# Performance work log

Measured on AMD Instinct MI355X. Metric: run time of the kernel, lower is better.

The kernel has to match this reference:

```python
import jax, jax.numpy as jnp
import numpy as np
import math


def _selective_scan(u, delta, A, Bs, Cs, D, delta_bias):
    """Mamba selective scan.
    u, delta: (B,K,Dn,L); A: (K,Dn,N); Bs, Cs: (B,K,N,L); D, delta_bias: (K,Dn).
    delta_softplus=True semantics from selective_scan_fn.
    """
    delta = jax.nn.softplus(delta + delta_bias[None, :, :, None])
    dl = jnp.moveaxis(delta, -1, 0)  # (L,B,K,Dn)
    ul = jnp.moveaxis(u, -1, 0)      # (L,B,K,Dn)
    bl = jnp.moveaxis(Bs, -1, 0)     # (L,B,K,N)
    cl = jnp.moveaxis(Cs, -1, 0)     # (L,B,K,N)
    h0 = jnp.zeros(u.shape[:3] + (A.shape[-1],), u.dtype)  # (B,K,Dn,N)

    def step(h, inp):
        d, ut, bt, ct = inp
        h = jnp.exp(d[..., None] * A) * h + (d * ut)[..., None] * bt[:, :, None, :]
        y = jnp.einsum('bkdn,bkn->bkd', h, ct)
        return h, y

    _, ys = jax.lax.scan(step, h0, (dl, ul, bl, cl))
    return jnp.moveaxis(ys, 0, -1) + D[None, :, :, None] * u  # (B,K,Dn,L)


def setup_inputs() -> dict:
    key = jax.random.key(0)
    B, H, W, C = 8, 64, 64, 192
    Dn, N, R, K = 192, 8, 12, 4
    ks = jax.random.split(key, 8)
    x = jax.random.normal(ks[0], (B, H, W, C), jnp.float32)
    in_proj_w = jax.random.normal(ks[1], (2 * Dn, C), jnp.float32) * (C ** -0.5)
    conv_w = jax.random.normal(ks[2], (Dn, 1, 3, 3), jnp.float32) * 0.2
    conv_b = jnp.zeros((Dn,), jnp.float32)
    x_proj_w = jax.random.normal(ks[3], (K, R + 2 * N, Dn), jnp.float32) * (Dn ** -0.5)
    dt_std = R ** -0.5
    dt_projs_w = jax.random.uniform(ks[4], (K, Dn, R), jnp.float32, -dt_std, dt_std)
    dt = jnp.exp(jax.random.uniform(ks[5], (K, Dn), jnp.float32)
                 * (math.log(0.1) - math.log(0.001)) + math.log(0.001))
    dt = jnp.clip(dt, 1e-4, None)
    dt_projs_b = dt + jnp.log(-jnp.expm1(-dt))  # inverse softplus
    A_logs = jnp.broadcast_to(jnp.log(jnp.arange(1, N + 1, dtype=jnp.float32)), (K, Dn, N)).copy()
    Ds = jnp.ones((K, Dn), jnp.float32)
    ln_w = jnp.ones((Dn,), jnp.float32)
    ln_b = jnp.zeros((Dn,), jnp.float32)
    out_proj_w = jax.random.normal(ks[6], (C, Dn), jnp.float32) * (Dn ** -0.5)
    return {"x": x, "in_proj_w": in_proj_w, "conv_w": conv_w, "conv_b": conv_b,
            "x_proj_w": x_proj_w, "dt_projs_w": dt_projs_w, "dt_projs_b": dt_projs_b,
            "A_logs": A_logs, "Ds": Ds, "ln_w": ln_w, "ln_b": ln_b,
            "out_proj_w": out_proj_w}


def reference(x, in_proj_w, conv_w, conv_b, x_proj_w, dt_projs_w, dt_projs_b,
              A_logs, Ds, ln_w, ln_b, out_proj_w):
    B, H, W, C = x.shape
    K, _, Dn = x_proj_w.shape
    N = A_logs.shape[-1]
    R = dt_projs_w.shape[-1]
    L = H * W

    xz = x @ in_proj_w.T                       # (B,H,W,2*Dn)
    xf, z = jnp.split(xz, 2, axis=-1)
    xc = jnp.transpose(xf, (0, 3, 1, 2))       # (B,Dn,H,W)
    xc = jax.lax.conv_general_dilated(
        xc, conv_w, (1, 1), [(1, 1), (1, 1)],
        feature_group_count=Dn,
        dimension_numbers=('NCHW', 'OIHW', 'NCHW')) + conv_b[None, :, None, None]
    xc = jax.nn.silu(xc)

    # 4-directional scan sequences: hw, wh, reversed-hw, reversed-wh
    x_hw = xc.reshape(B, Dn, L)
    x_wh = jnp.transpose(xc, (0, 1, 3, 2)).reshape(B, Dn, L)
    x2 = jnp.stack([x_hw, x_wh], axis=1)
    xs = jnp.concatenate([x2, jnp.flip(x2, axis=-1)], axis=1)  # (B,4,Dn,L)

    x_dbl = jnp.einsum('bkdl,kcd->bkcl', xs, x_proj_w)
    dts, Bsx, Csx = jnp.split(x_dbl, [R, R + N], axis=2)
    dts = jnp.einsum('bkrl,kdr->bkdl', dts, dt_projs_w)

    A = -jnp.exp(A_logs)                       # (K,Dn,N)
    out_y = _selective_scan(xs, dts, A, Bsx, Csx, Ds, dt_projs_b)  # (B,4,Dn,L)

    inv_y = jnp.flip(out_y[:, 2:4], axis=-1)
    wh_y = jnp.transpose(out_y[:, 1].reshape(B, Dn, W, H), (0, 1, 3, 2)).reshape(B, Dn, L)
    invwh_y = jnp.transpose(inv_y[:, 1].reshape(B, Dn, W, H), (0, 1, 3, 2)).reshape(B, Dn, L)
    y = out_y[:, 0] + inv_y[:, 0] + wh_y + invwh_y  # (B,Dn,L)

    y = jnp.transpose(y, (0, 2, 1)).reshape(B, H, W, Dn)
    mu = y.mean(-1, keepdims=True)
    var = y.var(-1, keepdims=True)
    y = (y - mu) / jnp.sqrt(var + 1e-5) * ln_w + ln_b
    y = y * jax.nn.silu(z)
    return y @ out_proj_w.T
```

## Files before the change

### kernel.cpp

```cpp
#include <hip/hip_runtime.h>
#include <hip/hip_bf16.h>

constexpr int B_  = 8;
constexpr int H_  = 64;
constexpr int W_  = 64;
constexpr int C_  = 192;
constexpr int Dn  = 192;
constexpr int Nst = 8;
constexpr int R_  = 12;
constexpr int K_  = 4;
constexpr int L_  = H_ * W_;
constexpr int CS  = 32;
constexpr int NC  = L_ / CS;
constexpr int CPROJ = R_ + 2 * Nst;
constexpr int MROWS = B_ * L_;

typedef __attribute__((ext_vector_type(8))) short short8v;
typedef __attribute__((ext_vector_type(4))) float f32x4;

__device__ __forceinline__ int map_t(int k, int t) {
    int tt = (k >= 2) ? (L_ - 1 - t) : t;
    if (k & 1) tt = (tt & 63) * 64 + (tt >> 6);
    return tt;
}

__device__ __forceinline__ short f2bf(float f) {
    unsigned u = __float_as_uint(f);
    u += 0x7FFFu + ((u >> 16) & 1u);
    return (short)(u >> 16);
}
__device__ __forceinline__ float bf2f(short s) {
    return __uint_as_float(((unsigned)(unsigned short)s) << 16);
}

constexpr int WOFF_IN  = 0;
constexpr int WOFF_XP  = 73728;
constexpr int WOFF_OUT = 95232;
constexpr int WTOTAL   = 132096;
constexpr int XUNITS   = MROWS * Dn / 8;
constexpr int WUNITS   = WTOTAL / 8;
__global__ __launch_bounds__(256) void k_cvt(const float* __restrict__ x,
                                             const float* __restrict__ w_in,
                                             const float* __restrict__ xpw,
                                             const float* __restrict__ wout,
                                             short* __restrict__ x_bf,
                                             short* __restrict__ w_bf) {
    int g = blockIdx.x * 256 + threadIdx.x;
    const float* src;
    short* dst;
    int off;
    if (g < XUNITS) { src = x; dst = x_bf; off = g * 8; }
    else {
        g -= XUNITS;
        if (g >= WUNITS) return;
        int base = g * 8;
        dst = w_bf; off = base;
        if (base < WOFF_XP)       { src = w_in; }
        else if (base < WOFF_OUT) { src = xpw;  src -= WOFF_XP; }
        else                      { src = wout; src -= WOFF_OUT; }
    }
    float4 a = *reinterpret_cast<const float4*>(src + off);
    float4 b = *reinterpret_cast<const float4*>(src + off + 4);
    short8v v = {f2bf(a.x), f2bf(a.y), f2bf(a.z), f2bf(a.w),
                 f2bf(b.x), f2bf(b.y), f2bf(b.z), f2bf(b.w)};
    *reinterpret_cast<short8v*>(dst + off) = v;
}

__device__ __forceinline__ void mgemm_core(const short* __restrict__ A,
                                           const short* __restrict__ Wb,
                                           f32x4 (&acc)[4][2],
                                           int mrow, int ncol, int Nact, int K) {
    const int lane = threadIdx.x & 63;
    const int koff = (lane >> 4) * 8;
    for (int k0 = 0; k0 < K; k0 += 32) {
        short8v af[4], bfr[2];
#pragma unroll
        for (int mf = 0; mf < 4; mf++)
            af[mf] = *reinterpret_cast<const short8v*>(
                A + (size_t)(mrow + mf * 16) * K + k0 + koff);
#pragma unroll
        for (int nf = 0; nf < 2; nf++) {
            int r = ncol + nf * 16;
            short8v z = {0, 0, 0, 0, 0, 0, 0, 0};
            bfr[nf] = (r < Nact)
                ? *reinterpret_cast<const short8v*>(Wb + (size_t)r * K + k0 + koff)
                : z;
        }
#pragma unroll
        for (int mf = 0; mf < 4; mf++)
#pragma unroll
            for (int nf = 0; nf < 2; nf++)
                acc[mf][nf] = __builtin_amdgcn_mfma_f32_16x16x32_bf16(
                    af[mf], bfr[nf], acc[mf][nf], 0, 0, 0);
    }
}

__global__ __launch_bounds__(256) void k_mgemm_f(const short* __restrict__ A,
                                                 const short* __restrict__ Wb,
                                                 float* __restrict__ out0,
                                                 int Nact, int K) {
    const int m0 = blockIdx.x * 128, n0 = blockIdx.y * 64;
    const int wid = threadIdx.x >> 6, lane = threadIdx.x & 63;
    const int wm = wid >> 1, wn = wid & 1;
    f32x4 acc[4][2] = {};
    mgemm_core(A, Wb, acc, m0 + wm * 64 + (lane & 15), n0 + wn * 32 + (lane & 15),
               Nact, K);
    const int prow = (lane >> 4) * 4, pcol = lane & 15;
#pragma unroll
    for (int mf = 0; mf < 4; mf++) {
        int mbase = m0 + wm * 64 + mf * 16 + prow;
#pragma unroll
        for (int nf = 0; nf < 2; nf++) {
            int n = n0 + wn * 32 + nf * 16 + pcol;
            if (n >= Nact) continue;
#pragma unroll
            for (int r = 0; r < 4; r++)
                out0[(size_t)(mbase + r) * Nact + n] = acc[mf][nf][r];
        }
    }
}

__global__ __launch_bounds__(256) void k_mgemm_in(const short* __restrict__ A,
                                                  const short* __restrict__ Wb,
                                                  short* __restrict__ xf_bf,
                                                  short* __restrict__ z_bf,
                                                  int K) {
    const int m0 = blockIdx.x * 128, n0 = blockIdx.y * 64;
    const int wid = threadIdx.x >> 6, lane = threadIdx.x & 63;
    const int wm = wid >> 1, wn = wid & 1;
    f32x4 acc[4][2] = {};
    mgemm_core(A, Wb, acc, m0 + wm * 64 + (lane & 15), n0 + wn * 32 + (lane & 15),
               384, K);
    const int prow = (lane >> 4) * 4, pcol = lane & 15;
#pragma unroll
    for (int mf = 0; mf < 4; mf++) {
        int mbase = m0 + wm * 64 + mf * 16 + prow;
#pragma unroll
        for (int nf = 0; nf < 2; nf++) {
            int n = n0 + wn * 32 + nf * 16 + pcol;
#pragma unroll
            for (int r = 0; r < 4; r++) {
                int m = mbase + r;
                if (n < 192) xf_bf[(size_t)m * 192 + n] = f2bf(acc[mf][nf][r]);
                else         z_bf[(size_t)m * 192 + (n - 192)] = f2bf(acc[mf][nf][r]);
            }
        }
    }
}

__global__ __launch_bounds__(256) void k_conv(const short* __restrict__ xfb,
                                              const float* __restrict__ cw,
                                              const float* __restrict__ cb,
                                              short* __restrict__ xcb) {
    size_t i = (size_t)blockIdx.x * 256 + threadIdx.x;
    int d = (int)(i % Dn);
    int p = (int)(i / Dn);
    int w = p & 63; p >>= 6;
    int h = p & 63; p >>= 6;
    int b = p;
    float acc = cb[d];
#pragma unroll
    for (int kh = 0; kh < 3; kh++) {
        int hh = h + kh - 1;
        if (hh < 0 || hh >= H_) continue;
#pragma unroll
        for (int kw = 0; kw < 3; kw++) {
            int ww = w + kw - 1;
            if (ww < 0 || ww >= W_) continue;
            acc = fmaf(bf2f(xfb[(((size_t)b * H_ + hh) * W_ + ww) * Dn + d]),
                       cw[d * 9 + kh * 3 + kw], acc);
        }
    }
    float sig = 1.f / (1.f + __expf(-acc));
    xcb[i] = f2bf(acc * sig);
}

__device__ __forceinline__ void delta_e1(float x, float& delta, float& e1) {
    if (x > 20.f) { delta = x; e1 = __expf(-x); }
    else {
        float t = __expf(x);
        delta = __logf(1.f + t);
        e1 = __builtin_amdgcn_rcpf(1.f + t);
    }
}

__device__ __forceinline__ float dot12(const float4& a, const float4& b,
                                       const float4& c, const float* w, float x) {
    x = fmaf(a.x, w[0], x);  x = fmaf(a.y, w[1], x);
    x = fmaf(a.z, w[2], x);  x = fmaf(a.w, w[3], x);
    x = fmaf(b.x, w[4], x);  x = fmaf(b.y, w[5], x);
    x = fmaf(b.z, w[6], x);  x = fmaf(b.w, w[7], x);
    x = fmaf(c.x, w[8], x);  x = fmaf(c.y, w[9], x);
    x = fmaf(c.z, w[10], x); x = fmaf(c.w, w[11], x);
    return x;
}

__global__ __launch_bounds__(192) void k_scan1(const short* __restrict__ xcb,
                                               const float* __restrict__ xdbl,
                                               const float* __restrict__ dtw_all,
                                               const float* __restrict__ dtb_all,
                                               const float* __restrict__ alog,
                                               float* __restrict__ Aprod,
                                               float* __restrict__ hpart) {
    const int blk = blockIdx.x;
    const int c = blk % NC;
    const int k = (blk / NC) % K_;
    const int b = blk / (NC * K_);
    const int d = threadIdx.x;
    const int t0 = c * CS;
    const int stride = ((k & 1) ? 64 : 1) * ((k >= 2) ? -1 : 1);
    const int lm0 = map_t(k, t0);

    __shared__ float4 sx4[CS][5];
    const float4* xd4 = reinterpret_cast<const float4*>(xdbl);
    for (int i = d; i < CS * 5; i += 192) {
        int ts = i / 5, q = i % 5;
        sx4[ts][q] = xd4[((size_t)b * L_ + lm0 + ts * stride) * 28 + k * 7 + q];
    }
    __syncthreads();

    float dtw[R_];
#pragma unroll
    for (int r = 0; r < R_; r++) dtw[r] = dtw_all[((size_t)k * Dn + d) * R_ + r];
    const float bias = dtb_all[k * Dn + d];
    float Av[Nst];
    bool fast = true;
#pragma unroll
    for (int n = 0; n < Nst; n++) {
        Av[n] = -__expf(alog[((size_t)k * Dn + d) * Nst + n]);
        fast = fast && (fabsf(Av[n] + (float)(n + 1)) < 1e-3f);
    }

    float h[Nst] = {};
    float Ap[Nst];
#pragma unroll
    for (int n = 0; n < Nst; n++) Ap[n] = 1.f;
    float e1p = 1.f;

    const long stepD = (long)stride * Dn;
    const short* up = xcb + ((size_t)b * L_ + lm0) * Dn + d;
    float u_next = bf2f(*up);
    if (fast) {
        for (int ts = 0; ts < CS; ts++) {
            float u = u_next;
            up += stepD;
            if (ts + 1 < CS) u_next = bf2f(*up);
            float4 q0 = sx4[ts][0], q1 = sx4[ts][1], q2 = sx4[ts][2];
            float4 qb0 = sx4[ts][3], qb1 = sx4[ts][4];
            float delta, e1; delta_e1(dot12(q0, q1, q2, dtw, bias), delta, e1);
            float du = delta * u;
            e1p *= e1;
            float a2 = e1 * e1, a3 = a2 * e1, a4 = a2 * a2;
            float a5 = a4 * e1, a6 = a4 * a2, a7 = a4 * a3, a8 = a4 * a4;
            h[0] = fmaf(e1, h[0], du * qb0.x);
            h[1] = fmaf(a2, h[1], du * qb0.y);
            h[2] = fmaf(a3, h[2], du * qb0.z);
            h[3] = fmaf(a4, h[3], du * qb0.w);
            h[4] = fmaf(a5, h[4], du * qb1.x);
            h[5] = fmaf(a6, h[5], du * qb1.y);
            h[6] = fmaf(a7, h[6], du * qb1.z);
            h[7] = fmaf(a8, h[7], du * qb1.w);
        }
        float p2 = e1p * e1p, p3 = p2 * e1p, p4 = p2 * p2;
        Ap[0] = e1p; Ap[1] = p2; Ap[2] = p3; Ap[3] = p4;
        Ap[4] = p4 * e1p; Ap[5] = p4 * p2; Ap[6] = p4 * p3; Ap[7] = p4 * p4;
    } else {
        for (int ts = 0; ts < CS; ts++) {
            float u = u_next;
            up += stepD;
            if (ts + 1 < CS) u_next = bf2f(*up);
            float4 q0 = sx4[ts][0], q1 = sx4[ts][1], q2 = sx4[ts][2];
            float4 qb0 = sx4[ts][3], qb1 = sx4[ts][4];
            float Bv[Nst] = {qb0.x, qb0.y, qb0.z, qb0.w, qb1.x, qb1.y, qb1.z, qb1.w};
            float delta, e1; delta_e1(dot12(q0, q1, q2, dtw, bias), delta, e1);
            float du = delta * u;
#pragma unroll
            for (int n = 0; n < Nst; n++) {
                float a = __expf(delta * Av[n]);
                Ap[n] *= a;
                h[n] = fmaf(a, h[n], du * Bv[n]);
            }
        }
    }
    size_t base = ((((size_t)(b * K_ + k) * NC + c) * Dn + d)) * Nst;
#pragma unroll
    for (int n = 0; n < Nst; n++) { Aprod[base + n] = Ap[n]; hpart[base + n] = h[n]; }
}

__global__ __launch_bounds__(256) void k_scan2(const float* __restrict__ Aprod,
                                               const float* __restrict__ hpart,
                                               float* __restrict__ hin) {
    int idx = blockIdx.x * 256 + threadIdx.x;
    int dn = idx % (Dn * Nst);
    int bk = idx / (Dn * Nst);
    size_t stride = (size_t)Dn * Nst;
    size_t base = (size_t)bk * NC * stride + dn;
    float h = 0.f;
    for (int cc = 0; cc < NC; cc++) {
        size_t s = base + (size_t)cc * stride;
        hin[s] = h;
        h = fmaf(Aprod[s], h, hpart[s]);
    }
}

__global__ __launch_bounds__(192) void k_scan3(const short* __restrict__ xcb,
                                               const float* __restrict__ xdbl,
                                               const float* __restrict__ dtw_all,
                                               const float* __restrict__ dtb_all,
                                               const float* __restrict__ alog,
                                               const float* __restrict__ dvec,
                                               const float* __restrict__ hin,
                                               short* __restrict__ y0,
                                               short* __restrict__ y1,
                                               short* __restrict__ y2,
                                               short* __restrict__ y3) {
    const int blk = blockIdx.x;
    const int c = blk % NC;
    const int k = (blk / NC) % K_;
    const int b = blk / (NC * K_);
    const int d = threadIdx.x;
    const int t0 = c * CS;
    const int stride = ((k & 1) ? 64 : 1) * ((k >= 2) ? -1 : 1);
    const int lm0 = map_t(k, t0);
    short* __restrict__ yk = (k == 0) ? y0 : (k == 1) ? y1 : (k == 2) ? y2 : y3;

    __shared__ float4 sx4[CS][7];
    const float4* xd4 = reinterpret_cast<const float4*>(xdbl);
    for (int i = d; i < CS * 7; i += 192) {
        int ts = i / 7, q = i % 7;
        sx4[ts][q] = xd4[((size_t)b * L_ + lm0 + ts * stride) * 28 + k * 7 + q];
    }
    __syncthreads();

    float dtw[R_];
#pragma unroll
    for (int r = 0; r < R_; r++) dtw[r] = dtw_all[((size_t)k * Dn + d) * R_ + r];
    const float bias = dtb_all[k * Dn + d];
    const float Dk = dvec[k * Dn + d];
    float Av[Nst];
    bool fast = true;
#pragma unroll
    for (int n = 0; n < Nst; n++) {
        Av[n] = -__expf(alog[((size_t)k * Dn + d) * Nst + n]);
        fast = fast && (fabsf(Av[n] + (float)(n + 1)) < 1e-3f);
    }

    size_t hbase = ((((size_t)(b * K_ + k) * NC + c) * Dn + d)) * Nst;
    float h[Nst];
#pragma unroll
    for (int n = 0; n < Nst; n++) h[n] = hin[hbase + n];

    const long stepD = (long)stride * Dn;
    const short* up = xcb + ((size_t)b * L_ + lm0) * Dn + d;
    short* yp = yk + ((size_t)b * L_ + lm0) * Dn + d;
    float u_next = bf2f(*up);
    if (fast) {
        for (int ts = 0; ts < CS; ts++) {
            float u = u_next;
            up += stepD;
            if (ts + 1 < CS) u_next = bf2f(*up);
            float4 q0 = sx4[ts][0], q1 = sx4[ts][1], q2 = sx4[ts][2];
            float4 qb0 = sx4[ts][3], qb1 = sx4[ts][4];
            float4 qc0 = sx4[ts][5], qc1 = sx4[ts][6];
            float delta, e1; delta_e1(dot12(q0, q1, q2, dtw, bias), delta, e1);
            float du = delta * u;
            float a2 = e1 * e1, a3 = a2 * e1, a4 = a2 * a2;
            float a5 = a4 * e1, a6 = a4 * a2, a7 = a4 * a3, a8 = a4 * a4;
            h[0] = fmaf(e1, h[0], du * qb0.x);
            h[1] = fmaf(a2, h[1], du * qb0.y);
            h[2] = fmaf(a3, h[2], du * qb0.z);
            h[3] = fmaf(a4, h[3], du * qb0.w);
            h[4] = fmaf(a5, h[4], du * qb1.x);
            h[5] = fmaf(a6, h[5], du * qb1.y);
            h[6] = fmaf(a7, h[6], du * qb1.z);
            h[7] = fmaf(a8, h[7], du * qb1.w);
            float y = h[0] * qc0.x;
            y = fmaf(h[1], qc0.y, y);
            y = fmaf(h[2], qc0.z, y);
            y = fmaf(h[3], qc0.w, y);
            y = fmaf(h[4], qc1.x, y);
            y = fmaf(h[5], qc1.y, y);
            y = fmaf(h[6], qc1.z, y);
            y = fmaf(h[7], qc1.w, y);
            *yp = f2bf(fmaf(Dk, u, y));
            yp += stepD;
        }
    } else {
        for (int ts = 0; ts < CS; ts++) {
            float u = u_next;
            up += stepD;
            if (ts + 1 < CS) u_next = bf2f(*up);
            float4 q0 = sx4[ts][0], q1 = sx4[ts][1], q2 = sx4[ts][2];
            float4 qb0 = sx4[ts][3], qb1 = sx4[ts][4];
            float4 qc0 = sx4[ts][5], qc1 = sx4[ts][6];
            float Bv[Nst] = {qb0.x, qb0.y, qb0.z, qb0.w, qb1.x, qb1.y, qb1.z, qb1.w};
            float Cv[Nst] = {qc0.x, qc0.y, qc0.z, qc0.w, qc1.x, qc1.y, qc1.z, qc1.w};
            float delta, e1; delta_e1(dot12(q0, q1, q2, dtw, bias), delta, e1);
            float du = delta * u;
            float y = 0.f;
#pragma unroll
            for (int n = 0; n < Nst; n++) {
                float a = __expf(delta * Av[n]);
                h[n] = fmaf(a, h[n], du * Bv[n]);
                y = fmaf(h[n], Cv[n], y);
            }
            *yp = f2bf(fmaf(Dk, u, y));
            yp += stepD;
        }
    }
}

__global__ __launch_bounds__(256) void k_ln(const short* __restrict__ y0,
                                            const short* __restrict__ y1,
                                            const short* __restrict__ y2,
                                            const short* __restrict__ y3,
                                            const short* __restrict__ zb,
                                            const float* __restrict__ lnw,
                                            const float* __restrict__ lnb,
                                            short* __restrict__ yfin) {
    const int row = blockIdx.x * 4 + (threadIdx.x >> 6);
    const int lane = threadIdx.x & 63;
    const size_t base = (size_t)row * Dn;
    float v[3];
    float s = 0.f, s2 = 0.f;
#pragma unroll
    for (int j = 0; j < 3; j++) {
        size_t idx = base + lane + j * 64;
        v[j] = bf2f(y0[idx]) + bf2f(y1[idx]) + bf2f(y2[idx]) + bf2f(y3[idx]);
        s += v[j];
        s2 = fmaf(v[j], v[j], s2);
    }
#pragma unroll
    for (int o = 1; o < 64; o <<= 1) {
        s += __shfl_xor(s, o);
        s2 += __shfl_xor(s2, o);
    }
    const float inv = 1.f / 192.f;
    float mu = s * inv;
    float var = s2 * inv - mu * mu;
    float rstd = rsqrtf(var + 1e-5f);
#pragma unroll
    for (int j = 0; j < 3; j++) {
        int dd = lane + j * 64;
        size_t idx = base + dd;
        float zz = bf2f(zb[idx]);
        float sig = 1.f / (1.f + __expf(-zz));
        float res = ((v[j] - mu) * rstd * lnw[dd] + lnb[dd]) * (zz * sig);
        yfin[idx] = f2bf(res);
    }
}

extern "C" void kernel_launch(void* const* d_in, const int* in_sizes, int n_in,
                              void* d_out, int out_size, void* d_ws, size_t ws_size,
                              hipStream_t stream) {
    const float* x    = (const float*)d_in[0];
    const float* w_in = (const float*)d_in[1];
    const float* cw   = (const float*)d_in[2];
    const float* cb   = (const float*)d_in[3];
    const float* xpw  = (const float*)d_in[4];
    const float* dtw  = (const float*)d_in[5];
    const float* dtb  = (const float*)d_in[6];
    const float* alog = (const float*)d_in[7];
    const float* dvec = (const float*)d_in[8];
    const float* lnw  = (const float*)d_in[9];
    const float* lnb  = (const float*)d_in[10];
    const float* wout = (const float*)d_in[11];
    float* out = (float*)d_out;

    const size_t SH  = (size_t)MROWS * Dn;
    const size_t SCN = (size_t)B_ * K_ * NC * Dn * Nst;

    char* p = (char*)d_ws;
    short* x_bf  = (short*)p; p += SH * 2;
    short* xf_bf = (short*)p; p += SH * 2;
    short* z_bf  = (short*)p; p += SH * 2;
    short* xc_bf = (short*)p; p += SH * 2;
    float* xdbl  = (float*)p; p += (size_t)MROWS * (K_ * CPROJ) * 4;
    float* Aprod = (float*)p; p += SCN * 4;
    float* hpart = (float*)p; p += SCN * 4;
    float* hin   = (float*)p; p += SCN * 4;
    short* w_bf  = (short*)p;
    short* y0 = x_bf;
    short* y1 = xf_bf;
    short* y2 = (short*)Aprod;
    short* y3 = (short*)hpart;
    short* yfin_bf = (short*)hin;

    k_cvt<<<(XUNITS + WUNITS + 255) / 256, 256, 0, stream>>>(x, w_in, xpw, wout,
                                                             x_bf, w_bf);
    k_mgemm_in<<<dim3(MROWS / 128, 6), 256, 0, stream>>>(x_bf, w_bf + WOFF_IN,
                                                         xf_bf, z_bf, C_);
    k_conv<<<(int)(SH / 256), 256, 0, stream>>>(xf_bf, cw, cb, xc_bf);
    k_mgemm_f<<<dim3(MROWS / 128, 2), 256, 0, stream>>>(xc_bf, w_bf + WOFF_XP,
                                                        xdbl, K_ * CPROJ, Dn);
    k_scan1<<<B_ * K_ * NC, 192, 0, stream>>>(xc_bf, xdbl, dtw, dtb, alog, Aprod, hpart);
    k_scan2<<<(B_ * K_ * Dn * Nst) / 256, 256, 0, stream>>>(Aprod, hpart, hin);
    k_scan3<<<B_ * K_ * NC, 192, 0, stream>>>(xc_bf, xdbl, dtw, dtb, alog, dvec,
                                              hin, y0, y1, y2, y3);
    k_ln<<<MROWS / 4, 256, 0, stream>>>(y0, y1, y2, y3, z_bf, lnw, lnb, yfin_bf);
    k_mgemm_f<<<dim3(MROWS / 128, 3), 256, 0, stream>>>(yfin_bf, w_bf + WOFF_OUT,
                                                        out, C_, Dn);
}
```

Before: 237.7 us.

## Store x_dbl projection in bf16 and tighten scan arithmetic chains

The x_proj GEMM now writes its output in bf16 instead of fp32, halving the traffic that both scan kernels read when staging B/C/dt rows into shared memory, and the scans unpack the bf16 pairs on load. The softplus helper drops its branch in favour of a clamped exp, and the 12-term dt dot product and the C reduction are split into parallel accumulator chains to shorten dependency latency. Launch bounds hint an occupancy of 8 blocks. The cost is lower precision in delta, B and C, which feeds an exponential recurrence and may change accuracy.

```diff
diff --git a/kernel.cpp b/kernel.cpp
--- a/kernel.cpp
+++ b/kernel.cpp
@@ -120,6 +120,31 @@
     }
 }
 
+__global__ __launch_bounds__(256) void k_mgemm_b(const short* __restrict__ A,
+                                                 const short* __restrict__ Wb,
+                                                 short* __restrict__ out0,
+                                                 int Nact, int K) {
+    const int m0 = blockIdx.x * 128, n0 = blockIdx.y * 64;
+    const int wid = threadIdx.x >> 6, lane = threadIdx.x & 63;
+    const int wm = wid >> 1, wn = wid & 1;
+    f32x4 acc[4][2] = {};
+    mgemm_core(A, Wb, acc, m0 + wm * 64 + (lane & 15), n0 + wn * 32 + (lane & 15),
+               Nact, K);
+    const int prow = (lane >> 4) * 4, pcol = lane & 15;
+#pragma unroll
+    for (int mf = 0; mf < 4; mf++) {
+        int mbase = m0 + wm * 64 + mf * 16 + prow;
+#pragma unroll
+        for (int nf = 0; nf < 2; nf++) {
+            int n = n0 + wn * 32 + nf * 16 + pcol;
+            if (n >= Nact) continue;
+#pragma unroll
+            for (int r = 0; r < 4; r++)
+                out0[(size_t)(mbase + r) * Nact + n] = f2bf(acc[mf][nf][r]);
+        }
+    }
+}
+
 __global__ __launch_bounds__(256) void k_mgemm_in(const short* __restrict__ A,
                                                   const short* __restrict__ Wb,
                                                   short* __restrict__ xf_bf,
@@ -176,27 +201,31 @@
 }
 
 __device__ __forceinline__ void delta_e1(float x, float& delta, float& e1) {
-    if (x > 20.f) { delta = x; e1 = __expf(-x); }
-    else {
-        float t = __expf(x);
-        delta = __logf(1.f + t);
-        e1 = __builtin_amdgcn_rcpf(1.f + t);
-    }
-}
-
-__device__ __forceinline__ float dot12(const float4& a, const float4& b,
-                                       const float4& c, const float* w, float x) {
-    x = fmaf(a.x, w[0], x);  x = fmaf(a.y, w[1], x);
-    x = fmaf(a.z, w[2], x);  x = fmaf(a.w, w[3], x);
-    x = fmaf(b.x, w[4], x);  x = fmaf(b.y, w[5], x);
-    x = fmaf(b.z, w[6], x);  x = fmaf(b.w, w[7], x);
-    x = fmaf(c.x, w[8], x);  x = fmaf(c.y, w[9], x);
-    x = fmaf(c.z, w[10], x); x = fmaf(c.w, w[11], x);
-    return x;
-}
-
-__global__ __launch_bounds__(192) void k_scan1(const short* __restrict__ xcb,
-                                               const float* __restrict__ xdbl,
+    float t = __expf(fminf(x, 80.f));
+    float opt = 1.f + t;
+    delta = __logf(opt);
+    e1 = __builtin_amdgcn_rcpf(opt);
+}
+
+__device__ __forceinline__ float dot12t(const float4& a, const float4& b,
+                                        const float4& c, const float* w, float bias) {
+    float xa = fmaf(a.x, w[0], bias);
+    float xb = a.y * w[1];
+    float xc = a.z * w[2];
+    xa = fmaf(a.w, w[3], xa);
+    xb = fmaf(b.x, w[4], xb);
+    xc = fmaf(b.y, w[5], xc);
+    xa = fmaf(b.z, w[6], xa);
+    xb = fmaf(b.w, w[7], xb);
+    xc = fmaf(c.x, w[8], xc);
+    xa = fmaf(c.y, w[9], xa);
+    xb = fmaf(c.z, w[10], xb);
+    xc = fmaf(c.w, w[11], xc);
+    return (xa + xb) + xc;
+}
+
+__global__ __launch_bounds__(192, 8) void k_scan1(const short* __restrict__ xcb,
+                                               const unsigned* __restrict__ xdu,
                                                const float* __restrict__ dtw_all,
                                                const float* __restrict__ dtb_all,
                                                const float* __restrict__ alog,
@@ -212,10 +241,12 @@
     const int lm0 = map_t(k, t0);
 
     __shared__ float4 sx4[CS][5];
-    const float4* xd4 = reinterpret_cast<const float4*>(xdbl);
-    for (int i = d; i < CS * 5; i += 192) {
-        int ts = i / 5, q = i % 5;
-        sx4[ts][q] = xd4[((size_t)b * L_ + lm0 + ts * stride) * 28 + k * 7 + q];
+    for (int i = d; i < CS * 10; i += 192) {
+        int ts = i / 10, j = i % 10;
+        unsigned uv = xdu[((size_t)b * L_ + lm0 + ts * stride) * 56 + k * 14 + j];
+        float* row = reinterpret_cast<float*>(&sx4[ts][0]);
+        row[2 * j]     = bf2f((short)(uv & 0xffffu));
+        row[2 * j + 1] = bf2f((short)(uv >> 16));
     }
     __syncthreads();
 
@@ -247,7 +278,7 @@
             if (ts + 1 < CS) u_next = bf2f(*up);
             float4 q0 = sx4[ts][0], q1 = sx4[ts][1], q2 = sx4[ts][2];
             float4 qb0 = sx4[ts][3], qb1 = sx4[ts][4];
-            float delta, e1; delta_e1(dot12(q0, q1, q2, dtw, bias), delta, e1);
+            float delta, e1; delta_e1(dot12t(q0, q1, q2, dtw, bias), delta, e1);
             float du = delta * u;
             e1p *= e1;
             float a2 = e1 * e1, a3 = a2 * e1, a4 = a2 * a2;
@@ -272,7 +303,7 @@
             float4 q0 = sx4[ts][0], q1 = sx4[ts][1], q2 = sx4[ts][2];
             float4 qb0 = sx4[ts][3], qb1 = sx4[ts][4];
             float Bv[Nst] = {qb0.x, qb0.y, qb0.z, qb0.w, qb1.x, qb1.y, qb1.z, qb1.w};
-            float delta, e1; delta_e1(dot12(q0, q1, q2, dtw, bias), delta, e1);
+            float delta, e1; delta_e1(dot12t(q0, q1, q2, dtw, bias), delta, e1);
             float du = delta * u;
 #pragma unroll
             for (int n = 0; n < Nst; n++) {
@@ -303,8 +334,8 @@
     }
 }
 
-__global__ __launch_bounds__(192) void k_scan3(const short* __restrict__ xcb,
-                                               const float* __restrict__ xdbl,
+__global__ __launch_bounds__(192, 8) void k_scan3(const short* __restrict__ xcb,
+                                               const unsigned* __restrict__ xdu,
                                                const float* __restrict__ dtw_all,
                                                const float* __restrict__ dtb_all,
                                                const float* __restrict__ alog,
@@ -325,10 +356,12 @@
     short* __restrict__ yk = (k == 0) ? y0 : (k == 1) ? y1 : (k == 2) ? y2 : y3;
 
     __shared__ float4 sx4[CS][7];
-    const float4* xd4 = reinterpret_cast<const float4*>(xdbl);
-    for (int i = d; i < CS * 7; i += 192) {
-        int ts = i / 7, q = i % 7;
-        sx4[ts][q] = xd4[((size_t)b * L_ + lm0 + ts * stride) * 28 + k * 7 + q];
+    for (int i = d; i < CS * 14; i += 192) {
+        int ts = i / 14, j = i % 14;
+        unsigned uv = xdu[((size_t)b * L_ + lm0 + ts * stride) * 56 + k * 14 + j];
+        float* row = reinterpret_cast<float*>(&sx4[ts][0]);
+        row[2 * j]     = bf2f((short)(uv & 0xffffu));
+        row[2 * j + 1] = bf2f((short)(uv >> 16));
     }
     __syncthreads();
 
@@ -362,7 +395,7 @@
             float4 q0 = sx4[ts][0], q1 = sx4[ts][1], q2 = sx4[ts][2];
             float4 qb0 = sx4[ts][3], qb1 = sx4[ts][4];
             float4 qc0 = sx4[ts][5], qc1 = sx4[ts][6];
-            float delta, e1; delta_e1(dot12(q0, q1, q2, dtw, bias), delta, e1);
+            float delta, e1; delta_e1(dot12t(q0, q1, q2, dtw, bias), delta, e1);
             float du = delta * u;
             float a2 = e1 * e1, a3 = a2 * e1, a4 = a2 * a2;
             float a5 = a4 * e1, a6 = a4 * a2, a7 = a4 * a3, a8 = a4 * a4;
@@ -374,15 +407,15 @@
             h[5] = fmaf(a6, h[5], du * qb1.y);
             h[6] = fmaf(a7, h[6], du * qb1.z);
             h[7] = fmaf(a8, h[7], du * qb1.w);
-            float y = h[0] * qc0.x;
-            y = fmaf(h[1], qc0.y, y);
-            y = fmaf(h[2], qc0.z, y);
-            y = fmaf(h[3], qc0.w, y);
-            y = fmaf(h[4], qc1.x, y);
-            y = fmaf(h[5], qc1.y, y);
-            y = fmaf(h[6], qc1.z, y);
-            y = fmaf(h[7], qc1.w, y);
-            *yp = f2bf(fmaf(Dk, u, y));
+            float ya = fmaf(h[0], qc0.x, Dk * u);
+            float yb = h[4] * qc1.x;
+            ya = fmaf(h[1], qc0.y, ya);
+            yb = fmaf(h[5], qc1.y, yb);
+            ya = fmaf(h[2], qc0.z, ya);
+            yb = fmaf(h[6], qc1.z, yb);
+            ya = fmaf(h[3], qc0.w, ya);
+            yb = fmaf(h[7], qc1.w, yb);
+            *yp = f2bf(ya + yb);
             yp += stepD;
         }
     } else {
@@ -395,16 +428,16 @@
             float4 qc0 = sx4[ts][5], qc1 = sx4[ts][6];
             float Bv[Nst] = {qb0.x, qb0.y, qb0.z, qb0.w, qb1.x, qb1.y, qb1.z, qb1.w};
             float Cv[Nst] = {qc0.x, qc0.y, qc0.z, qc0.w, qc1.x, qc1.y, qc1.z, qc1.w};
-            float delta, e1; delta_e1(dot12(q0, q1, q2, dtw, bias), delta, e1);
+            float delta, e1; delta_e1(dot12t(q0, q1, q2, dtw, bias), delta, e1);
             float du = delta * u;
-            float y = 0.f;
+            float y = Dk * u;
 #pragma unroll
             for (int n = 0; n < Nst; n++) {
                 float a = __expf(delta * Av[n]);
                 h[n] = fmaf(a, h[n], du * Bv[n]);
                 y = fmaf(h[n], Cv[n], y);
             }
-            *yp = f2bf(fmaf(Dk, u, y));
+            *yp = f2bf(y);
             yp += stepD;
         }
     }
@@ -475,7 +508,7 @@
     short* xf_bf = (short*)p; p += SH * 2;
     short* z_bf  = (short*)p; p += SH * 2;
     short* xc_bf = (short*)p; p += SH * 2;
-    float* xdbl  = (float*)p; p += (size_t)MROWS * (K_ * CPROJ) * 4;
+    short* xdbl_bf = (short*)p; p += (size_t)MROWS * (K_ * CPROJ) * 2;
     float* Aprod = (float*)p; p += SCN * 4;
     float* hpart = (float*)p; p += SCN * 4;
     float* hin   = (float*)p; p += SCN * 4;
@@ -485,17 +518,18 @@
     short* y2 = (short*)Aprod;
     short* y3 = (short*)hpart;
     short* yfin_bf = (short*)hin;
+    const unsigned* xdu = (const unsigned*)xdbl_bf;
 
     k_cvt<<<(XUNITS + WUNITS + 255) / 256, 256, 0, stream>>>(x, w_in, xpw, wout,
                                                              x_bf, w_bf);
     k_mgemm_in<<<dim3(MROWS / 128, 6), 256, 0, stream>>>(x_bf, w_bf + WOFF_IN,
                                                          xf_bf, z_bf, C_);
     k_conv<<<(int)(SH / 256), 256, 0, stream>>>(xf_bf, cw, cb, xc_bf);
-    k_mgemm_f<<<dim3(MROWS / 128, 2), 256, 0, stream>>>(xc_bf, w_bf + WOFF_XP,
-                                                        xdbl, K_ * CPROJ, Dn);
-    k_scan1<<<B_ * K_ * NC, 192, 0, stream>>>(xc_bf, xdbl, dtw, dtb, alog, Aprod, hpart);
+    k_mgemm_b<<<dim3(MROWS / 128, 2), 256, 0, stream>>>(xc_bf, w_bf + WOFF_XP,
+                                                        xdbl_bf, K_ * CPROJ, Dn);
+    k_scan1<<<B_ * K_ * NC, 192, 0, stream>>>(xc_bf, xdu, dtw, dtb, alog, Aprod, hpart);
     k_scan2<<<(B_ * K_ * Dn * Nst) / 256, 256, 0, stream>>>(Aprod, hpart, hin);
-    k_scan3<<<B_ * K_ * NC, 192, 0, stream>>>(xc_bf, xdbl, dtw, dtb, alog, dvec,
+    k_scan3<<<B_ * K_ * NC, 192, 0, stream>>>(xc_bf, xdu, dtw, dtb, alog, dvec,
                                               hin, y0, y1, y2, y3);
     k_ln<<<MROWS / 4, 256, 0, stream>>>(y0, y1, y2, y3, z_bf, lnw, lnb, yfin_bf);
     k_mgemm_f<<<dim3(MROWS / 128, 3), 256, 0, stream>>>(yfin_bf, w_bf + WOFF_OUT,
```

Result: slower. 243.3 us (+2.3%).
